# Performance work log

Hardware: AMD Instinct MI355X
Metric: run time of the kernel (lower is better)

The kernel has to match this reference:

```python
import jax, jax.numpy as jnp
import numpy as np

D_MODEL, D_FF, N_LAYERS, N_EXPERTS = 512, 1024, 2, 8
TOP_K, TEMP = 2, 1.0
B, S = 2, 1024


def _ln(x, g, b, eps=1e-5):
    m = x.mean(-1, keepdims=True)
    v = x.var(-1, keepdims=True)
    return (x - m) / jnp.sqrt(v + eps) * g + b


def setup_inputs() -> dict:
    key = jax.random.key(0)
    ks = jax.random.split(key, 32)
    s = 0.02
    rn = lambda k, sh: jax.random.normal(k, sh, jnp.float32) * s
    E, D, F, L = N_EXPERTS, D_MODEL, D_FF, N_LAYERS
    return {
        'x': jax.random.normal(ks[0], (B, S, D), jnp.float32),
        # policy head: Linear(D, D//2) -> LN -> GELU -> Linear(D//2, E)
        'pw1': rn(ks[1], (D, D // 2)), 'pb1': jnp.zeros((D // 2,)),
        'pg1': jnp.ones((D // 2,)), 'pbb1': jnp.zeros((D // 2,)),
        'pw2': rn(ks[2], (D // 2, E)), 'pb2': jnp.zeros((E,)),
        # stacked expert params [E, ...]
        'Win': rn(ks[3], (E, D, F)), 'b_in': jnp.zeros((E, F)),
        'W1': rn(ks[4], (E, L, F, 2 * F)), 'b1': jnp.zeros((E, L, 2 * F)),
        'W2': rn(ks[5], (E, L, 2 * F, F)), 'b2': jnp.zeros((E, L, F)),
        'ng': jnp.ones((E, L, F)), 'nb': jnp.zeros((E, L, F)),
        'gw': rn(ks[6], (E, L, F)),
        'Wout': rn(ks[7], (E, F, D)), 'bout': jnp.zeros((E, D)),
        'fng': jnp.ones((E, D)), 'fnb': jnp.zeros((E, D)),
    }


def reference(x, pw1, pb1, pg1, pbb1, pw2, pb2,
              Win, b_in, W1, b1, W2, b2, ng, nb, gw, Wout, bout, fng, fnb):
    # policy logits [B,S,E]
    h = _ln(x @ pw1 + pb1, pg1, pbb1)
    logits = (jax.nn.gelu(h, approximate=False) @ pw2 + pb2) / TEMP
    # Gumbel-top-k routing (fixed noise key for determinism)
    u = jax.random.uniform(jax.random.key(42), logits.shape, logits.dtype)
    g = -jnp.log(-jnp.log(u + 1e-10) + 1e-10)
    scores = logits + g
    _, idx = jax.lax.top_k(scores, TOP_K)              # [B,S,K]
    sel = (idx[..., None] == jnp.arange(N_EXPERTS)).any(axis=-2)  # [B,S,E]

    def expert(Win_e, bin_e, W1_e, b1_e, W2_e, b2_e, ng_e, nb_e, gw_e,
               Wout_e, bout_e, fng_e, fnb_e):
        h = x @ Win_e + bin_e                          # [B,S,F]
        for l in range(N_LAYERS):
            h2 = jax.nn.gelu(h @ W1_e[l] + b1_e[l], approximate=False)
            h2 = h2 @ W2_e[l] + b2_e[l]
            h2 = _ln(h2, ng_e[l], nb_e[l])
            gate = jax.nn.sigmoid(h @ gw_e[l][:, None])  # [B,S,1]
            h = h + gate * h2
        out = h @ Wout_e + bout_e
        return _ln(x + out, fng_e, fnb_e)              # [B,S,D]

    eouts = jax.vmap(expert)(Win, b_in, W1, b1, W2, b2, ng, nb, gw,
                             Wout, bout, fng, fnb)     # [E,B,S,D]
    # combine: torch code sums (unweighted) expert outputs over selected experts
    outputs = jnp.einsum('ebsd,bse->bsd', eouts, sel.astype(x.dtype))
    return outputs
```

## Files before the change

### kernel.cpp

```cpp
#include <hip/hip_runtime.h>
#include <hip/hip_bf16.h>

#define N_EXP   8
#define NTOK    2048
#define TOTROWS 4096
#define PTOK    4

typedef __hip_bfloat16 bf16;
typedef __attribute__((ext_vector_type(8))) short short8;
typedef __attribute__((ext_vector_type(4))) float floatx4;

#define TN 128
#define TK 32
#define LDAB 40


__device__ inline float gelu_f(float v) {
    return 0.5f * v * (1.0f + erff(v * 0.70710678118654752440f));
}

__device__ inline float block_sum256(float v, float* red) {
    #pragma unroll
    for (int off = 32; off > 0; off >>= 1)
        v += __shfl_down(v, off, 64);
    __syncthreads();
    if ((threadIdx.x & 63) == 0) red[threadIdx.x >> 6] = v;
    __syncthreads();
    return red[0] + red[1] + red[2] + red[3];
}

__device__ inline unsigned rotl32(unsigned v, int d) { return (v << d) | (v >> (32 - d)); }

__device__ inline void threefry2x32(unsigned k0, unsigned k1, unsigned x0, unsigned x1,
                                    unsigned& o0, unsigned& o1) {
    unsigned ks2 = k0 ^ k1 ^ 0x1BD11BDAu;
    x0 += k0; x1 += k1;
#define TF_R(r) { x0 += x1; x1 = rotl32(x1, r); x1 ^= x0; }
    TF_R(13) TF_R(15) TF_R(26) TF_R(6)
    x0 += k1; x1 += ks2 + 1u;
    TF_R(17) TF_R(29) TF_R(16) TF_R(24)
    x0 += ks2; x1 += k0 + 2u;
    TF_R(13) TF_R(15) TF_R(26) TF_R(6)
    x0 += k0; x1 += k1 + 3u;
    TF_R(17) TF_R(29) TF_R(16) TF_R(24)
    x0 += k1; x1 += ks2 + 4u;
    TF_R(13) TF_R(15) TF_R(26) TF_R(6)
    x0 += ks2; x1 += k0 + 5u;
#undef TF_R
    o0 = x0; o1 = x1;
}

__device__ inline int expert_of(int r, const int* bases) {
    int e = 0;
    #pragma unroll
    for (int i = 1; i < N_EXP; ++i) if (r >= bases[i]) e = i;
    return e;
}


__global__ __launch_bounds__(256) void policy_k(
    const float* __restrict__ x, const float* __restrict__ pw1,
    const float* __restrict__ pb1, const float* __restrict__ pg1,
    const float* __restrict__ pbb1, const float* __restrict__ pw2,
    const float* __restrict__ pb2, int2* __restrict__ top2, int* __restrict__ counts)
{
    const int tb  = blockIdx.x * PTOK;
    const int lid = threadIdx.x;
    __shared__ float xs[PTOK][512];
    __shared__ float hbs[PTOK][256];
    __shared__ float red[4];
    __shared__ float sc[PTOK][8];

    {
        const float4* xp = (const float4*)(x + (long long)tb * 512);
        float4* xsp = (float4*)&xs[0][0];
        xsp[lid]       = xp[lid];
        xsp[lid + 256] = xp[lid + 256];
    }
    __syncthreads();

    float av[PTOK];
    {
        float b0 = pb1[lid];
        #pragma unroll
        for (int tt = 0; tt < PTOK; ++tt) av[tt] = b0;
    }
    #pragma unroll 4
    for (int d = 0; d < 512; ++d) {
        float w = pw1[d * 256 + lid];
        #pragma unroll
        for (int tt = 0; tt < PTOK; ++tt)
            av[tt] = fmaf(xs[tt][d], w, av[tt]);
    }

    #pragma unroll
    for (int tt = 0; tt < PTOK; ++tt) {
        float s  = block_sum256(av[tt], red);
        float sq = block_sum256(av[tt] * av[tt], red);
        float mean = s * (1.0f / 256.0f);
        float var  = sq * (1.0f / 256.0f) - mean * mean;
        float rstd = rsqrtf(var + 1e-5f);
        float hn = (av[tt] - mean) * rstd * pg1[lid] + pbb1[lid];
        hbs[tt][lid] = gelu_f(hn);
    }
    __syncthreads();

    if (lid < PTOK * 8) {
        const int tt = lid >> 3;
        const int e  = lid & 7;
        float lg = pb2[e];
        for (int j = 0; j < 256; ++j)
            lg = fmaf(hbs[tt][j], pw2[j * 8 + e], lg);
        unsigned idx = (unsigned)(tb + tt) * 8u + (unsigned)e;
        unsigned o0, o1;
        threefry2x32(0u, 42u, 0u, idx, o0, o1);
        unsigned bits = o0 ^ o1;
        float u = __uint_as_float((bits >> 9) | 0x3f800000u) - 1.0f;
        float gml = -logf(-logf(u + 1e-10f) + 1e-10f);
        sc[tt][e] = lg + gml;
    }
    __syncthreads();
    if (lid < PTOK) {
        float b0 = -INFINITY; int i0 = 0;
        #pragma unroll
        for (int e = 0; e < 8; ++e) if (sc[lid][e] > b0) { b0 = sc[lid][e]; i0 = e; }
        float b1v = -INFINITY; int i1 = 0;
        #pragma unroll
        for (int e = 0; e < 8; ++e) if (e != i0 && sc[lid][e] > b1v) { b1v = sc[lid][e]; i1 = e; }
        top2[tb + lid] = make_int2(i0, i1);
        atomicAdd(&counts[i0], 1);
        atomicAdd(&counts[i1], 1);
    }
}

__global__ void prefix_k(const int* __restrict__ counts, int* __restrict__ cursor,
                         int* __restrict__ bases) {
    if (threadIdx.x == 0 && blockIdx.x == 0) {
        int s = 0;
        for (int e = 0; e < N_EXP; ++e) { bases[e] = s; cursor[e] = s; s += counts[e]; }
    }
}

__global__ __launch_bounds__(256) void scatter_k(const int2* __restrict__ top2,
                                                 int* __restrict__ cursor,
                                                 int* __restrict__ list) {
    int t = blockIdx.x * 256 + threadIdx.x;
    int2 p = top2[t];
    int pos = atomicAdd(&cursor[p.x], 1); list[pos] = t;
    pos     = atomicAdd(&cursor[p.y], 1); list[pos] = t;
}


__global__ __launch_bounds__(256) void cast_x_k(const float* __restrict__ x,
                                                bf16* __restrict__ xb) {
    int i = (blockIdx.x * 256 + threadIdx.x) * 4;
    float4 v = *(const float4*)(x + i);
    bf16 o[4] = { (bf16)v.x, (bf16)v.y, (bf16)v.z, (bf16)v.w };
    *(unsigned long long*)(xb + i) = *(unsigned long long*)o;
}


template <typename CT, int TMp>
__global__ __launch_bounds__(256) void mgemm_k(
    const bf16* __restrict__ A, const int* __restrict__ gather,
    const float* __restrict__ W, long long westride,
    const float* __restrict__ bias, int bestride,
    CT* __restrict__ C, bf16* __restrict__ Cmir,
    const int* __restrict__ counts, const int* __restrict__ bases,
    int K, int N, int act)
{
    const int e   = blockIdx.z;
    const int cnt = counts[e];
    const int m0  = blockIdx.y * TMp;
    if (m0 >= cnt) return;
    const int rbase = bases[e];
    const int n0  = blockIdx.x * TN;
    const float* We = W + (long long)e * westride;

    constexpr int MI = TMp / 32;

    __shared__ __align__(16) unsigned short As[2][TMp * LDAB];
    __shared__ __align__(16) unsigned short Bs[2][TN * LDAB];

    const int tid  = threadIdx.x;
    const int lane = tid & 63;
    const int wv   = tid >> 6;
    const int wm   = (wv & 1) * (TMp / 2);
    const int wn   = (wv >> 1) * 64;
    const int q    = lane >> 4;
    const int ln   = lane & 15;

    const int ar = tid >> 2;
    const int ak = (tid & 3) * 8;
    long long arow0 = 0, arow1 = 0;
    {
        int r0 = m0 + ar; if (r0 > cnt - 1) r0 = cnt - 1;
        long long p0 = gather ? (long long)gather[rbase + r0] : (long long)(rbase + r0);
        arow0 = p0 * K;
        if (TMp == 128) {
            int r1 = m0 + 64 + ar; if (r1 > cnt - 1) r1 = cnt - 1;
            long long p1 = gather ? (long long)gather[rbase + r1] : (long long)(rbase + r1);
            arow1 = p1 * K;
        }
    }
    const int bn  = (wv & 1) * 64 + lane;
    const int bkb = (wv >> 1) * 16;
    const float* wcol = We + n0 + bn;

    floatx4 acc[MI][4];
    #pragma unroll
    for (int i = 0; i < MI; ++i)
        #pragma unroll
        for (int j = 0; j < 4; ++j)
            acc[i][j] = (floatx4){0.f, 0.f, 0.f, 0.f};

    uint4 a0A = {0,0,0,0}, a1A = {0,0,0,0}, a0B = {0,0,0,0}, a1B = {0,0,0,0};
    float wA[16], wB[16];

    auto mg_load = [&](uint4& a0r, uint4& a1r, float (&wr)[16], int koff) {
        a0r = *(const uint4*)(A + arow0 + koff + ak);
        if (TMp == 128) a1r = *(const uint4*)(A + arow1 + koff + ak);
        const float* wp = wcol + (long long)(koff + bkb) * N;
        #pragma unroll
        for (int kk = 0; kk < 16; ++kk) wr[kk] = wp[(long long)kk * N];
    };
    auto mg_store = [&](const uint4& a0r, const uint4& a1r, const float (&wr)[16], int buf) {
        *(uint4*)(&As[buf][ar * LDAB + ak]) = a0r;
        if (TMp == 128) *(uint4*)(&As[buf][(64 + ar) * LDAB + ak]) = a1r;
        union { unsigned short us[8]; uint4 v; } p0, p1;
        #pragma unroll
        for (int kk = 0; kk < 8; ++kk) {
            bf16 b0 = (bf16)wr[kk];
            bf16 b1 = (bf16)wr[kk + 8];
            p0.us[kk] = *(unsigned short*)&b0;
            p1.us[kk] = *(unsigned short*)&b1;
        }
        *(uint4*)(&Bs[buf][bn * LDAB + bkb])     = p0.v;
        *(uint4*)(&Bs[buf][bn * LDAB + bkb + 8]) = p1.v;
    };
    auto mg_compute = [&](int buf) {
        short8 a_frag[MI], b_frag[4];
        #pragma unroll
        for (int i = 0; i < MI; ++i)
            a_frag[i] = *(const short8*)(&As[buf][(wm + i * 16 + ln) * LDAB + q * 8]);
        #pragma unroll
        for (int j = 0; j < 4; ++j)
            b_frag[j] = *(const short8*)(&Bs[buf][(wn + j * 16 + ln) * LDAB + q * 8]);
        #pragma unroll
        for (int i = 0; i < MI; ++i)
            #pragma unroll
            for (int j = 0; j < 4; ++j)
                acc[i][j] = __builtin_amdgcn_mfma_f32_16x16x32_bf16(
                    a_frag[i], b_frag[j], acc[i][j], 0, 0, 0);
    };

    mg_load(a0A, a1A, wA, 0);
    mg_store(a0A, a1A, wA, 0);
    mg_load(a0B, a1B, wB, TK);
    __syncthreads();

    int k0 = 0;
    for (; k0 + 2 * TK < K; k0 += 2 * TK) {
        mg_load(a0A, a1A, wA, k0 + 2 * TK);
        mg_compute(0);
        mg_store(a0B, a1B, wB, 1);
        __syncthreads();
        mg_load(a0B, a1B, wB, k0 + 3 * TK);
        mg_compute(1);
        mg_store(a0A, a1A, wA, 0);
        __syncthreads();
    }
    mg_compute(0);
    mg_store(a0B, a1B, wB, 1);
    __syncthreads();
    mg_compute(1);

    #pragma unroll
    for (int i = 0; i < MI; ++i) {
        int rbase_i = m0 + wm + i * 16 + q * 4;
        #pragma unroll
        for (int j = 0; j < 4; ++j) {
            int n = n0 + wn + j * 16 + ln;
            float bv = bias[e * bestride + n];
            #pragma unroll
            for (int rg = 0; rg < 4; ++rg) {
                int r = rbase_i + rg;
                if (r >= cnt) continue;
                float v = acc[i][j][rg] + bv;
                if (act) v = gelu_f(v);
                long long off = (long long)(rbase + r) * N + n;
                C[off] = (CT)v;
                if (Cmir) Cmir[off] = (bf16)v;
            }
        }
    }
}


__global__ __launch_bounds__(256) void lngate_k(
    float* __restrict__ h, bf16* __restrict__ hb, const float* __restrict__ h2,
    const float* __restrict__ ng, const float* __restrict__ nb,
    const float* __restrict__ gw, const int* __restrict__ bases, int l)
{
    const int r = blockIdx.x;
    const int e = expert_of(r, bases);
    const int lid = threadIdx.x;
    const float* hr  = h  + (long long)r * 1024;
    const float* h2r = h2 + (long long)r * 1024;
    const int off = (e * 2 + l) * 1024;
    __shared__ float red[4];

    float s = 0.f, sq = 0.f, dt = 0.f;
    float hv[4], h2v[4];
    #pragma unroll
    for (int i = 0; i < 4; ++i) {
        int j = lid + 256 * i;
        float a = h2r[j];
        float b = hr[j];
        hv[i] = b; h2v[i] = a;
        s += a; sq += a * a;
        dt = fmaf(b, gw[off + j], dt);
    }
    s  = block_sum256(s, red);
    sq = block_sum256(sq, red);
    dt = block_sum256(dt, red);
    float mean = s * (1.f / 1024.f);
    float rstd = rsqrtf(sq * (1.f / 1024.f) - mean * mean + 1e-5f);
    float gate = 1.f / (1.f + expf(-dt));
    float* hw  = h  + (long long)r * 1024;
    bf16*  hbw = hb + (long long)r * 1024;
    #pragma unroll
    for (int i = 0; i < 4; ++i) {
        int j = lid + 256 * i;
        float v = (h2v[i] - mean) * rstd * ng[off + j] + nb[off + j];
        float nh = hv[i] + gate * v;
        hw[j] = nh;
        hbw[j] = (bf16)nh;
    }
}


__global__ __launch_bounds__(256) void final_k(
    const float* __restrict__ x, const bf16* __restrict__ orow,
    const float* __restrict__ fng, const float* __restrict__ fnb,
    const int* __restrict__ bases, const int* __restrict__ list,
    float* __restrict__ out)
{
    const int r = blockIdx.x;
    const int e = expert_of(r, bases);
    const int t = list[r];
    const int lid = threadIdx.x;
    __shared__ float red[4];

    float y[2];
    float s = 0.f, sq = 0.f;
    #pragma unroll
    for (int i = 0; i < 2; ++i) {
        int j = lid + 256 * i;
        float v = x[(long long)t * 512 + j] + (float)orow[(long long)r * 512 + j];
        y[i] = v; s += v; sq += v * v;
    }
    s  = block_sum256(s, red);
    sq = block_sum256(sq, red);
    float mean = s * (1.f / 512.f);
    float rstd = rsqrtf(sq * (1.f / 512.f) - mean * mean + 1e-5f);
    #pragma unroll
    for (int i = 0; i < 2; ++i) {
        int j = lid + 256 * i;
        float v = (y[i] - mean) * rstd * fng[e * 512 + j] + fnb[e * 512 + j];
        atomicAdd(&out[(long long)t * 512 + j], v);
    }
}


extern "C" void kernel_launch(void* const* d_in, const int* in_sizes, int n_in,
                              void* d_out, int out_size, void* d_ws, size_t ws_size,
                              hipStream_t stream) {
    const float* x    = (const float*)d_in[0];
    const float* pw1  = (const float*)d_in[1];
    const float* pb1  = (const float*)d_in[2];
    const float* pg1  = (const float*)d_in[3];
    const float* pbb1 = (const float*)d_in[4];
    const float* pw2  = (const float*)d_in[5];
    const float* pb2  = (const float*)d_in[6];
    const float* Win  = (const float*)d_in[7];
    const float* b_in = (const float*)d_in[8];
    const float* W1   = (const float*)d_in[9];
    const float* b1   = (const float*)d_in[10];
    const float* W2   = (const float*)d_in[11];
    const float* b2   = (const float*)d_in[12];
    const float* ng   = (const float*)d_in[13];
    const float* nb   = (const float*)d_in[14];
    const float* gw   = (const float*)d_in[15];
    const float* Wout = (const float*)d_in[16];
    const float* bout = (const float*)d_in[17];
    const float* fng  = (const float*)d_in[18];
    const float* fnb  = (const float*)d_in[19];
    float* out = (float*)d_out;
    (void)ws_size; (void)in_sizes; (void)n_in;

    char* ws = (char*)d_ws;
    int* counts = (int*)ws;
    int* cursor = counts + 8;
    int* bases  = cursor + 8;
    int2* top2  = (int2*)(ws + 128);
    int*  list  = (int*)(ws + 128 + 2048 * 8);
    size_t o = 128 + 2048 * 8 + 4096 * 4;
    o = (o + 255) & ~(size_t)255;
    bf16*  xb   = (bf16*) (ws + o); o += (size_t)NTOK * 512 * 2;
    float* h    = (float*)(ws + o); o += (size_t)TOTROWS * 1024 * 4;
    bf16*  hb   = (bf16*) (ws + o); o += (size_t)TOTROWS * 1024 * 2;
    bf16*  tb   = (bf16*) (ws + o); o += (size_t)TOTROWS * 2048 * 2;
    float* h2   = (float*)(ws + o); o += (size_t)TOTROWS * 1024 * 4;
    bf16*  orow = (bf16*) (ws + o); o += (size_t)TOTROWS * 512 * 2;

    hipMemsetAsync(d_out, 0, (size_t)out_size * sizeof(float), stream);
    hipMemsetAsync(ws, 0, 64, stream);

    policy_k<<<NTOK / PTOK, 256, 0, stream>>>(x, pw1, pb1, pg1, pbb1, pw2, pb2, top2, counts);
    prefix_k<<<1, 64, 0, stream>>>(counts, cursor, bases);
    scatter_k<<<NTOK / 256, 256, 0, stream>>>(top2, cursor, list);
    cast_x_k<<<NTOK * 512 / 1024, 256, 0, stream>>>(x, xb);

    mgemm_k<float, 64><<<dim3(8, 32, 8), 256, 0, stream>>>(
        xb, list, Win, (long long)512 * 1024, b_in, 1024, h, hb,
        counts, bases, 512, 1024, 0);

    for (int l = 0; l < 2; ++l) {
        mgemm_k<bf16, 64><<<dim3(16, 32, 8), 256, 0, stream>>>(
            hb, nullptr, W1 + (long long)l * 1024 * 2048, (long long)2 * 1024 * 2048,
            b1 + l * 2048, 2 * 2048, tb, (bf16*)nullptr,
            counts, bases, 1024, 2048, 1);
        mgemm_k<float, 64><<<dim3(8, 32, 8), 256, 0, stream>>>(
            tb, nullptr, W2 + (long long)l * 2048 * 1024, (long long)2 * 2048 * 1024,
            b2 + l * 1024, 2 * 1024, h2, (bf16*)nullptr,
            counts, bases, 2048, 1024, 0);
        lngate_k<<<TOTROWS, 256, 0, stream>>>(h, hb, h2, ng, nb, gw, bases, l);
    }

    mgemm_k<bf16, 64><<<dim3(4, 32, 8), 256, 0, stream>>>(
        hb, nullptr, Wout, (long long)1024 * 512, bout, 512, orow, (bf16*)nullptr,
        counts, bases, 1024, 512, 0);

    final_k<<<TOTROWS, 256, 0, stream>>>(x, orow, fng, fnb, bases, list, out);
}
```

Measured before the change: 805.8 us.

## Pre-transpose expert weights to bf16 and use 128-row tiles for FFN GEMMs

```diff
diff --git a/kernel.cpp b/kernel.cpp
--- a/kernel.cpp
+++ b/kernel.cpp
@@ -160,10 +160,45 @@
 }
 
 
-template <typename CT, int TMp>
+__global__ __launch_bounds__(256) void wcast_k(const float* __restrict__ in,
+                                               bf16* __restrict__ outp,
+                                               int R, int C, int tiles_r)
+{
+    const int mt = blockIdx.x;
+    const long long b = blockIdx.y;
+    const int tr = mt % tiles_r;
+    const int tc = mt / tiles_r;
+    const int r0 = tr * 64, c0 = tc * 64;
+    __shared__ unsigned short t[64 * 80];
+    const int tid = threadIdx.x;
+    const int rr = tid >> 4;
+    const int cc = (tid & 15) * 4;
+    const float* inb = in + ((long long)b * R + r0) * (long long)C + c0;
+    #pragma unroll
+    for (int i = 0; i < 4; ++i) {
+        int r = rr + 16 * i;
+        float4 v = *(const float4*)(inb + (long long)r * C + cc);
+        bf16 x0 = (bf16)v.x, x1 = (bf16)v.y, x2 = (bf16)v.z, x3 = (bf16)v.w;
+        t[(cc + 0) * 80 + r] = *(unsigned short*)&x0;
+        t[(cc + 1) * 80 + r] = *(unsigned short*)&x1;
+        t[(cc + 2) * 80 + r] = *(unsigned short*)&x2;
+        t[(cc + 3) * 80 + r] = *(unsigned short*)&x3;
+    }
+    __syncthreads();
+    const int cr = tid >> 2;
+    const int rk = (tid & 3) * 16;
+    bf16* ob = outp + ((long long)b * C + c0 + cr) * (long long)R + r0 + rk;
+    uint4 w0 = *(const uint4*)(&t[cr * 80 + rk]);
+    uint4 w1 = *(const uint4*)(&t[cr * 80 + rk + 8]);
+    *(uint4*)(ob)     = w0;
+    *(uint4*)(ob + 8) = w1;
+}
+
+
+template <typename CT, int TMp, bool BT>
 __global__ __launch_bounds__(256) void mgemm_k(
     const bf16* __restrict__ A, const int* __restrict__ gather,
-    const float* __restrict__ W, long long westride,
+    const float* __restrict__ W, const bf16* __restrict__ WT, long long westride,
     const float* __restrict__ bias, int bestride,
     CT* __restrict__ C, bf16* __restrict__ Cmir,
     const int* __restrict__ counts, const int* __restrict__ bases,
@@ -175,7 +210,6 @@
     if (m0 >= cnt) return;
     const int rbase = bases[e];
     const int n0  = blockIdx.x * TN;
-    const float* We = W + (long long)e * westride;
 
     constexpr int MI = TMp / 32;
 
@@ -205,7 +239,9 @@
     }
     const int bn  = (wv & 1) * 64 + lane;
     const int bkb = (wv >> 1) * 16;
-    const float* wcol = We + n0 + bn;
+    const float* wcol = BT ? nullptr : (W + (long long)e * westride + n0 + bn);
+    const bf16*  wtcol = BT ? (WT + (long long)e * westride
+                               + (long long)(n0 + bn) * K + bkb) : nullptr;
 
     floatx4 acc[MI][4];
     #pragma unroll
@@ -214,29 +250,42 @@
         for (int j = 0; j < 4; ++j)
             acc[i][j] = (floatx4){0.f, 0.f, 0.f, 0.f};
 
-    uint4 a0A = {0,0,0,0}, a1A = {0,0,0,0}, a0B = {0,0,0,0}, a1B = {0,0,0,0};
+    uint4 aA0 = {0,0,0,0}, aA1 = {0,0,0,0}, aB0 = {0,0,0,0}, aB1 = {0,0,0,0};
+    uint4 bA0 = {0,0,0,0}, bA1 = {0,0,0,0}, bB0 = {0,0,0,0}, bB1 = {0,0,0,0};
     float wA[16], wB[16];
 
-    auto mg_load = [&](uint4& a0r, uint4& a1r, float (&wr)[16], int koff) {
+    auto mg_load = [&](uint4& a0r, uint4& a1r, uint4& b0r, uint4& b1r,
+                       float (&wr)[16], int koff) {
         a0r = *(const uint4*)(A + arow0 + koff + ak);
         if (TMp == 128) a1r = *(const uint4*)(A + arow1 + koff + ak);
-        const float* wp = wcol + (long long)(koff + bkb) * N;
-        #pragma unroll
-        for (int kk = 0; kk < 16; ++kk) wr[kk] = wp[(long long)kk * N];
+        if constexpr (BT) {
+            b0r = *(const uint4*)(wtcol + koff);
+            b1r = *(const uint4*)(wtcol + koff + 8);
+        } else {
+            const float* wp = wcol + (long long)(koff + bkb) * N;
+            #pragma unroll
+            for (int kk = 0; kk < 16; ++kk) wr[kk] = wp[(long long)kk * N];
+        }
     };
-    auto mg_store = [&](const uint4& a0r, const uint4& a1r, const float (&wr)[16], int buf) {
+    auto mg_store = [&](const uint4& a0r, const uint4& a1r, const uint4& b0r,
+                        const uint4& b1r, const float (&wr)[16], int buf) {
         *(uint4*)(&As[buf][ar * LDAB + ak]) = a0r;
         if (TMp == 128) *(uint4*)(&As[buf][(64 + ar) * LDAB + ak]) = a1r;
-        union { unsigned short us[8]; uint4 v; } p0, p1;
-        #pragma unroll
-        for (int kk = 0; kk < 8; ++kk) {
-            bf16 b0 = (bf16)wr[kk];
-            bf16 b1 = (bf16)wr[kk + 8];
-            p0.us[kk] = *(unsigned short*)&b0;
-            p1.us[kk] = *(unsigned short*)&b1;
+        if constexpr (BT) {
+            *(uint4*)(&Bs[buf][bn * LDAB + bkb])     = b0r;
+            *(uint4*)(&Bs[buf][bn * LDAB + bkb + 8]) = b1r;
+        } else {
+            union { unsigned short us[8]; uint4 v; } p0, p1;
+            #pragma unroll
+            for (int kk = 0; kk < 8; ++kk) {
+                bf16 c0 = (bf16)wr[kk];
+                bf16 c1 = (bf16)wr[kk + 8];
+                p0.us[kk] = *(unsigned short*)&c0;
+                p1.us[kk] = *(unsigned short*)&c1;
+            }
+            *(uint4*)(&Bs[buf][bn * LDAB + bkb])     = p0.v;
+            *(uint4*)(&Bs[buf][bn * LDAB + bkb + 8]) = p1.v;
         }
-        *(uint4*)(&Bs[buf][bn * LDAB + bkb])     = p0.v;
-        *(uint4*)(&Bs[buf][bn * LDAB + bkb + 8]) = p1.v;
     };
     auto mg_compute = [&](int buf) {
         short8 a_frag[MI], b_frag[4];
@@ -254,24 +303,24 @@
                     a_frag[i], b_frag[j], acc[i][j], 0, 0, 0);
     };
 
-    mg_load(a0A, a1A, wA, 0);
-    mg_store(a0A, a1A, wA, 0);
-    mg_load(a0B, a1B, wB, TK);
+    mg_load(aA0, aA1, bA0, bA1, wA, 0);
+    mg_store(aA0, aA1, bA0, bA1, wA, 0);
+    mg_load(aB0, aB1, bB0, bB1, wB, TK);
     __syncthreads();
 
     int k0 = 0;
     for (; k0 + 2 * TK < K; k0 += 2 * TK) {
-        mg_load(a0A, a1A, wA, k0 + 2 * TK);
+        mg_load(aA0, aA1, bA0, bA1, wA, k0 + 2 * TK);
         mg_compute(0);
-        mg_store(a0B, a1B, wB, 1);
+        mg_store(aB0, aB1, bB0, bB1, wB, 1);
         __syncthreads();
-        mg_load(a0B, a1B, wB, k0 + 3 * TK);
+        mg_load(aB0, aB1, bB0, bB1, wB, k0 + 3 * TK);
         mg_compute(1);
-        mg_store(a0A, a1A, wA, 0);
+        mg_store(aA0, aA1, bA0, bA1, wA, 0);
         __syncthreads();
     }
     mg_compute(0);
-    mg_store(a0B, a1B, wB, 1);
+    mg_store(aB0, aB1, bB0, bB1, wB, 1);
     __syncthreads();
     mg_compute(1);
 
@@ -413,6 +462,12 @@
     bf16*  tb   = (bf16*) (ws + o); o += (size_t)TOTROWS * 2048 * 2;
     float* h2   = (float*)(ws + o); o += (size_t)TOTROWS * 1024 * 4;
     bf16*  orow = (bf16*) (ws + o); o += (size_t)TOTROWS * 512 * 2;
+    o = (o + 255) & ~(size_t)255;
+    bf16* Wint  = (bf16*)(ws + o); o += (size_t)8 * 1024 * 512 * 2;
+    bf16* W1t   = (bf16*)(ws + o); o += (size_t)8 * 2 * 2048 * 1024 * 2;
+    bf16* W2t   = (bf16*)(ws + o); o += (size_t)8 * 2 * 1024 * 2048 * 2;
+    bf16* Woutt = (bf16*)(ws + o); o += (size_t)8 * 512 * 1024 * 2;
+    const bool bt = (o <= ws_size);
 
     hipMemsetAsync(d_out, 0, (size_t)out_size * sizeof(float), stream);
     hipMemsetAsync(ws, 0, 64, stream);
@@ -422,25 +477,50 @@
     scatter_k<<<NTOK / 256, 256, 0, stream>>>(top2, cursor, list);
     cast_x_k<<<NTOK * 512 / 1024, 256, 0, stream>>>(x, xb);
 
-    mgemm_k<float, 64><<<dim3(8, 32, 8), 256, 0, stream>>>(
-        xb, list, Win, (long long)512 * 1024, b_in, 1024, h, hb,
-        counts, bases, 512, 1024, 0);
-
-    for (int l = 0; l < 2; ++l) {
-        mgemm_k<bf16, 64><<<dim3(16, 32, 8), 256, 0, stream>>>(
-            hb, nullptr, W1 + (long long)l * 1024 * 2048, (long long)2 * 1024 * 2048,
-            b1 + l * 2048, 2 * 2048, tb, (bf16*)nullptr,
-            counts, bases, 1024, 2048, 1);
-        mgemm_k<float, 64><<<dim3(8, 32, 8), 256, 0, stream>>>(
-            tb, nullptr, W2 + (long long)l * 2048 * 1024, (long long)2 * 2048 * 1024,
-            b2 + l * 1024, 2 * 1024, h2, (bf16*)nullptr,
-            counts, bases, 2048, 1024, 0);
-        lngate_k<<<TOTROWS, 256, 0, stream>>>(h, hb, h2, ng, nb, gw, bases, l);
-    }
-
-    mgemm_k<bf16, 64><<<dim3(4, 32, 8), 256, 0, stream>>>(
-        hb, nullptr, Wout, (long long)1024 * 512, bout, 512, orow, (bf16*)nullptr,
-        counts, bases, 1024, 512, 0);
+    if (bt) {
+        wcast_k<<<dim3(128, 8),  256, 0, stream>>>(Win,  Wint,  512,  1024, 8);
+        wcast_k<<<dim3(512, 16), 256, 0, stream>>>(W1,   W1t,   1024, 2048, 16);
+        wcast_k<<<dim3(512, 16), 256, 0, stream>>>(W2,   W2t,   2048, 1024, 32);
+        wcast_k<<<dim3(128, 8),  256, 0, stream>>>(Wout, Woutt, 1024, 512,  16);
+
+        mgemm_k<float, 64, true><<<dim3(8, 32, 8), 256, 0, stream>>>(
+            xb, list, nullptr, Wint, (long long)512 * 1024, b_in, 1024, h, hb,
+            counts, bases, 512, 1024, 0);
+
+        for (int l = 0; l < 2; ++l) {
+            mgemm_k<bf16, 128, true><<<dim3(16, 16, 8), 256, 0, stream>>>(
+                hb, nullptr, nullptr, W1t + (long long)l * 2048 * 1024,
+                (long long)2 * 2048 * 1024, b1 + l * 2048, 2 * 2048, tb, (bf16*)nullptr,
+                counts, bases, 1024, 2048, 1);
+            mgemm_k<float, 128, true><<<dim3(8, 16, 8), 256, 0, stream>>>(
+                tb, nullptr, nullptr, W2t + (long long)l * 1024 * 2048,
+                (long long)2 * 1024 * 2048, b2 + l * 1024, 2 * 1024, h2, (bf16*)nullptr,
+                counts, bases, 2048, 1024, 0);
+            lngate_k<<<TOTROWS, 256, 0, stream>>>(h, hb, h2, ng, nb, gw, bases, l);
+        }
+
+        mgemm_k<bf16, 64, true><<<dim3(4, 32, 8), 256, 0, stream>>>(
+            hb, nullptr, nullptr, Woutt, (long long)512 * 1024, bout, 512, orow,
+            (bf16*)nullptr, counts, bases, 1024, 512, 0);
+    } else {
+        mgemm_k<float, 64, false><<<dim3(8, 32, 8), 256, 0, stream>>>(
+            xb, list, Win, nullptr, (long long)512 * 1024, b_in, 1024, h, hb,
+            counts, bases, 512, 1024, 0);
+        for (int l = 0; l < 2; ++l) {
+            mgemm_k<bf16, 128, false><<<dim3(16, 16, 8), 256, 0, stream>>>(
+                hb, nullptr, W1 + (long long)l * 1024 * 2048, nullptr,
+                (long long)2 * 1024 * 2048, b1 + l * 2048, 2 * 2048, tb, (bf16*)nullptr,
+                counts, bases, 1024, 2048, 1);
+            mgemm_k<float, 128, false><<<dim3(8, 16, 8), 256, 0, stream>>>(
+                tb, nullptr, W2 + (long long)l * 2048 * 1024, nullptr,
+                (long long)2 * 2048 * 1024, b2 + l * 1024, 2 * 1024, h2, (bf16*)nullptr,
+                counts, bases, 2048, 1024, 0);
+            lngate_k<<<TOTROWS, 256, 0, stream>>>(h, hb, h2, ng, nb, gw, bases, l);
+        }
+        mgemm_k<bf16, 64, false><<<dim3(4, 32, 8), 256, 0, stream>>>(
+            hb, nullptr, Wout, nullptr, (long long)1024 * 512, bout, 512, orow,
+            (bf16*)nullptr, counts, bases, 1024, 512, 0);
+    }
 
     final_k<<<TOTROWS, 256, 0, stream>>>(x, orow, fng, fnb, bases, list, out);
 }
```

After: 886.8 us. +10.1%, slower.

## Pre-cast weights to swizzled bf16 tiles and stage GEMM operands via direct global-to-LDS loads

Applied to the files above, without the earlier changes.

```diff
diff --git a/kernel.cpp b/kernel.cpp
--- a/kernel.cpp
+++ b/kernel.cpp
@@ -10,13 +10,15 @@
 typedef __attribute__((ext_vector_type(8))) short short8;
 typedef __attribute__((ext_vector_type(4))) float floatx4;
 
-#define TN 128
-#define TK 32
-#define LDAB 40
-
 
 __device__ inline float gelu_f(float v) {
     return 0.5f * v * (1.0f + erff(v * 0.70710678118654752440f));
+}
+
+__device__ __forceinline__ void gll16(const void* g, void* l) {
+    __builtin_amdgcn_global_load_lds(
+        (__attribute__((address_space(1))) void*)g,
+        (__attribute__((address_space(3))) void*)l, 16, 0, 0);
 }
 
 __device__ inline float block_sum256(float v, float* red) {
@@ -160,10 +162,55 @@
 }
 
 
+__global__ __launch_bounds__(256) void wcast_k(const float* __restrict__ in,
+                                               bf16* __restrict__ outp,
+                                               int K, int N, int tiles_k)
+{
+    const int mt = blockIdx.x;
+    const long long b = blockIdx.y;
+    const int tk = mt % tiles_k;
+    const int tn = mt / tiles_k;
+    const int k0 = tk * 64, n0c = tn * 64;
+    __shared__ unsigned short t[64 * 80];
+    const int tid = threadIdx.x;
+    const int rr = tid >> 4;
+    const int cc = (tid & 15) * 4;
+    const float* inb = in + ((long long)b * K + k0) * (long long)N + n0c;
+    #pragma unroll
+    for (int i = 0; i < 4; ++i) {
+        int r = rr + 16 * i;
+        float4 v = *(const float4*)(inb + (long long)r * N + cc);
+        bf16 x0 = (bf16)v.x, x1 = (bf16)v.y, x2 = (bf16)v.z, x3 = (bf16)v.w;
+        t[(cc + 0) * 80 + r] = *(unsigned short*)&x0;
+        t[(cc + 1) * 80 + r] = *(unsigned short*)&x1;
+        t[(cc + 2) * 80 + r] = *(unsigned short*)&x2;
+        t[(cc + 3) * 80 + r] = *(unsigned short*)&x3;
+    }
+    __syncthreads();
+    const int nl = tid >> 2;
+    const int ks = (tid & 3) * 16;
+    const int n  = n0c + nl;
+    const int nprime = n & 127;
+    const int nt = n >> 7;
+    const int NT = N >> 7, KT = K >> 5;
+    const int swz = (nprime >> 1) & 3;
+    #pragma unroll
+    for (int u = 0; u < 2; ++u) {
+        int k  = k0 + ks + u * 8;
+        int kt = k >> 5;
+        int ch = (k >> 3) & 3;
+        int chs = ch ^ swz;
+        long long off = ((((long long)b * NT + nt) * KT + kt) << 12)
+                        + (nprime << 5) + (chs << 3);
+        *(uint4*)(outp + off) = *(const uint4*)(&t[nl * 80 + ks + u * 8]);
+    }
+}
+
+
 template <typename CT, int TMp>
 __global__ __launch_bounds__(256) void mgemm_k(
     const bf16* __restrict__ A, const int* __restrict__ gather,
-    const float* __restrict__ W, long long westride,
+    const bf16* __restrict__ WT, long long westride,
     const float* __restrict__ bias, int bestride,
     CT* __restrict__ C, bf16* __restrict__ Cmir,
     const int* __restrict__ counts, const int* __restrict__ bases,
@@ -174,13 +221,15 @@
     const int m0  = blockIdx.y * TMp;
     if (m0 >= cnt) return;
     const int rbase = bases[e];
-    const int n0  = blockIdx.x * TN;
-    const float* We = W + (long long)e * westride;
+    const int nt  = blockIdx.x;
+    const int n0  = nt * 128;
+    const int KT  = K >> 5;
 
     constexpr int MI = TMp / 32;
-
-    __shared__ __align__(16) unsigned short As[2][TMp * LDAB];
-    __shared__ __align__(16) unsigned short Bs[2][TN * LDAB];
+    constexpr int AI = TMp / 64;
+
+    __shared__ __align__(16) char As[2][TMp * 64];
+    __shared__ __align__(16) char Bs[2][128 * 64];
 
     const int tid  = threadIdx.x;
     const int lane = tid & 63;
@@ -189,23 +238,19 @@
     const int wn   = (wv >> 1) * 64;
     const int q    = lane >> 4;
     const int ln   = lane & 15;
-
-    const int ar = tid >> 2;
-    const int ak = (tid & 3) * 8;
-    long long arow0 = 0, arow1 = 0;
-    {
-        int r0 = m0 + ar; if (r0 > cnt - 1) r0 = cnt - 1;
-        long long p0 = gather ? (long long)gather[rbase + r0] : (long long)(rbase + r0);
-        arow0 = p0 * K;
-        if (TMp == 128) {
-            int r1 = m0 + 64 + ar; if (r1 > cnt - 1) r1 = cnt - 1;
-            long long p1 = gather ? (long long)gather[rbase + r1] : (long long)(rbase + r1);
-            arow1 = p1 * K;
-        }
-    }
-    const int bn  = (wv & 1) * 64 + lane;
-    const int bkb = (wv >> 1) * 16;
-    const float* wcol = We + n0 + bn;
+    const int qsw  = q ^ ((ln >> 1) & 3);
+
+    long long aoff[AI];
+    #pragma unroll
+    for (int i = 0; i < AI; ++i) {
+        int rt = wv * (TMp / 4) + i * 16 + (lane >> 2);
+        int r  = m0 + rt; if (r > cnt - 1) r = cnt - 1;
+        long long rowp = gather ? (long long)gather[rbase + r] : (long long)(rbase + r);
+        int sc = (lane & 3) ^ ((rt >> 1) & 3);
+        aoff[i] = rowp * K + sc * 8;
+    }
+    const bf16* bsrc = WT + (long long)e * westride + (long long)nt * KT * 4096
+                       + wv * 1024 + lane * 8;
 
     floatx4 acc[MI][4];
     #pragma unroll
@@ -214,38 +259,23 @@
         for (int j = 0; j < 4; ++j)
             acc[i][j] = (floatx4){0.f, 0.f, 0.f, 0.f};
 
-    uint4 a0A = {0,0,0,0}, a1A = {0,0,0,0}, a0B = {0,0,0,0}, a1B = {0,0,0,0};
-    float wA[16], wB[16];
-
-    auto mg_load = [&](uint4& a0r, uint4& a1r, float (&wr)[16], int koff) {
-        a0r = *(const uint4*)(A + arow0 + koff + ak);
-        if (TMp == 128) a1r = *(const uint4*)(A + arow1 + koff + ak);
-        const float* wp = wcol + (long long)(koff + bkb) * N;
-        #pragma unroll
-        for (int kk = 0; kk < 16; ++kk) wr[kk] = wp[(long long)kk * N];
+    auto STAGE = [&](int buf, int kt) {
+        const int k0 = kt << 5;
+        #pragma unroll
+        for (int i = 0; i < AI; ++i)
+            gll16(A + aoff[i] + k0, &As[buf][wv * (TMp * 16) + i * 1024]);
+        const bf16* bs = bsrc + (long long)kt * 4096;
+        gll16(bs,       &Bs[buf][wv * 2048]);
+        gll16(bs + 512, &Bs[buf][wv * 2048 + 1024]);
     };
-    auto mg_store = [&](const uint4& a0r, const uint4& a1r, const float (&wr)[16], int buf) {
-        *(uint4*)(&As[buf][ar * LDAB + ak]) = a0r;
-        if (TMp == 128) *(uint4*)(&As[buf][(64 + ar) * LDAB + ak]) = a1r;
-        union { unsigned short us[8]; uint4 v; } p0, p1;
-        #pragma unroll
-        for (int kk = 0; kk < 8; ++kk) {
-            bf16 b0 = (bf16)wr[kk];
-            bf16 b1 = (bf16)wr[kk + 8];
-            p0.us[kk] = *(unsigned short*)&b0;
-            p1.us[kk] = *(unsigned short*)&b1;
-        }
-        *(uint4*)(&Bs[buf][bn * LDAB + bkb])     = p0.v;
-        *(uint4*)(&Bs[buf][bn * LDAB + bkb + 8]) = p1.v;
-    };
-    auto mg_compute = [&](int buf) {
+    auto COMPUTE = [&](int buf) {
         short8 a_frag[MI], b_frag[4];
         #pragma unroll
         for (int i = 0; i < MI; ++i)
-            a_frag[i] = *(const short8*)(&As[buf][(wm + i * 16 + ln) * LDAB + q * 8]);
+            a_frag[i] = *(const short8*)(&As[buf][(wm + i * 16 + ln) * 64 + qsw * 16]);
         #pragma unroll
         for (int j = 0; j < 4; ++j)
-            b_frag[j] = *(const short8*)(&Bs[buf][(wn + j * 16 + ln) * LDAB + q * 8]);
+            b_frag[j] = *(const short8*)(&Bs[buf][(wn + j * 16 + ln) * 64 + qsw * 16]);
         #pragma unroll
         for (int i = 0; i < MI; ++i)
             #pragma unroll
@@ -254,26 +284,16 @@
                     a_frag[i], b_frag[j], acc[i][j], 0, 0, 0);
     };
 
-    mg_load(a0A, a1A, wA, 0);
-    mg_store(a0A, a1A, wA, 0);
-    mg_load(a0B, a1B, wB, TK);
-    __syncthreads();
-
-    int k0 = 0;
-    for (; k0 + 2 * TK < K; k0 += 2 * TK) {
-        mg_load(a0A, a1A, wA, k0 + 2 * TK);
-        mg_compute(0);
-        mg_store(a0B, a1B, wB, 1);
+    STAGE(0, 0);
+    __syncthreads();
+    int cur = 0;
+    for (int kt = 0; kt < KT - 1; ++kt) {
+        STAGE(cur ^ 1, kt + 1);
+        COMPUTE(cur);
         __syncthreads();
-        mg_load(a0B, a1B, wB, k0 + 3 * TK);
-        mg_compute(1);
-        mg_store(a0A, a1A, wA, 0);
-        __syncthreads();
-    }
-    mg_compute(0);
-    mg_store(a0B, a1B, wB, 1);
-    __syncthreads();
-    mg_compute(1);
+        cur ^= 1;
+    }
+    COMPUTE(cur);
 
     #pragma unroll
     for (int i = 0; i < MI; ++i) {
@@ -413,6 +433,11 @@
     bf16*  tb   = (bf16*) (ws + o); o += (size_t)TOTROWS * 2048 * 2;
     float* h2   = (float*)(ws + o); o += (size_t)TOTROWS * 1024 * 4;
     bf16*  orow = (bf16*) (ws + o); o += (size_t)TOTROWS * 512 * 2;
+    o = (o + 255) & ~(size_t)255;
+    bf16* Wint  = (bf16*)(ws + o); o += (size_t)8 * 1024 * 512 * 2;
+    bf16* W1t   = (bf16*)(ws + o); o += (size_t)8 * 2 * 2048 * 1024 * 2;
+    bf16* W2t   = (bf16*)(ws + o); o += (size_t)8 * 2 * 1024 * 2048 * 2;
+    bf16* Woutt = (bf16*)(ws + o); o += (size_t)8 * 512 * 1024 * 2;
 
     hipMemsetAsync(d_out, 0, (size_t)out_size * sizeof(float), stream);
     hipMemsetAsync(ws, 0, 64, stream);
@@ -422,24 +447,29 @@
     scatter_k<<<NTOK / 256, 256, 0, stream>>>(top2, cursor, list);
     cast_x_k<<<NTOK * 512 / 1024, 256, 0, stream>>>(x, xb);
 
+    wcast_k<<<dim3(8 * 16,  8),  256, 0, stream>>>(Win,  Wint,  512,  1024, 8);
+    wcast_k<<<dim3(16 * 32, 16), 256, 0, stream>>>(W1,   W1t,   1024, 2048, 16);
+    wcast_k<<<dim3(32 * 16, 16), 256, 0, stream>>>(W2,   W2t,   2048, 1024, 32);
+    wcast_k<<<dim3(16 * 8,  8),  256, 0, stream>>>(Wout, Woutt, 1024, 512,  16);
+
     mgemm_k<float, 64><<<dim3(8, 32, 8), 256, 0, stream>>>(
-        xb, list, Win, (long long)512 * 1024, b_in, 1024, h, hb,
+        xb, list, Wint, (long long)512 * 1024, b_in, 1024, h, hb,
         counts, bases, 512, 1024, 0);
 
     for (int l = 0; l < 2; ++l) {
-        mgemm_k<bf16, 64><<<dim3(16, 32, 8), 256, 0, stream>>>(
-            hb, nullptr, W1 + (long long)l * 1024 * 2048, (long long)2 * 1024 * 2048,
-            b1 + l * 2048, 2 * 2048, tb, (bf16*)nullptr,
+        mgemm_k<bf16, 128><<<dim3(16, 16, 8), 256, 0, stream>>>(
+            hb, nullptr, W1t + (long long)l * 2048 * 1024,
+            (long long)2 * 2048 * 1024, b1 + l * 2048, 2 * 2048, tb, (bf16*)nullptr,
             counts, bases, 1024, 2048, 1);
-        mgemm_k<float, 64><<<dim3(8, 32, 8), 256, 0, stream>>>(
-            tb, nullptr, W2 + (long long)l * 2048 * 1024, (long long)2 * 2048 * 1024,
-            b2 + l * 1024, 2 * 1024, h2, (bf16*)nullptr,
+        mgemm_k<float, 128><<<dim3(8, 16, 8), 256, 0, stream>>>(
+            tb, nullptr, W2t + (long long)l * 1024 * 2048,
+            (long long)2 * 1024 * 2048, b2 + l * 1024, 2 * 1024, h2, (bf16*)nullptr,
             counts, bases, 2048, 1024, 0);
         lngate_k<<<TOTROWS, 256, 0, stream>>>(h, hb, h2, ng, nb, gw, bases, l);
     }
 
     mgemm_k<bf16, 64><<<dim3(4, 32, 8), 256, 0, stream>>>(
-        hb, nullptr, Wout, (long long)1024 * 512, bout, 512, orow, (bf16*)nullptr,
+        hb, nullptr, Woutt, (long long)512 * 1024, bout, 512, orow, (bf16*)nullptr,
         counts, bases, 1024, 512, 0);
 
     final_k<<<TOTROWS, 256, 0, stream>>>(x, orow, fng, fnb, bases, list, out);
```

New measurement: 804.2 us. No clear change (-0.2%).
